# Optimization experiments

Measured on AMD Instinct MI355X. Metric: run time of the kernel, lower is better.

## Reference

```python
import jax, jax.numpy as jnp
import numpy as np


def setup_inputs() -> dict:
    key = jax.random.key(0)
    ks = jax.random.split(key, 8)
    C, dk = 256, 32
    B, H, W = 4, 64, 64
    x = jax.random.normal(ks[0], (B, C, H, W), dtype=jnp.float32)
    wq = jax.random.normal(ks[1], (dk, C), dtype=jnp.float32) * (1.0 / np.sqrt(C))
    bq = jnp.zeros((dk,), dtype=jnp.float32)
    wk = jax.random.normal(ks[2], (dk, C), dtype=jnp.float32) * (1.0 / np.sqrt(C))
    bk = jnp.zeros((dk,), dtype=jnp.float32)
    wv = jax.random.normal(ks[3], (C, C), dtype=jnp.float32) * (1.0 / np.sqrt(C))
    bv = jnp.zeros((C,), dtype=jnp.float32)
    gamma = jnp.ones((1,), dtype=jnp.float32)
    return {"x": x, "wq": wq, "bq": bq, "wk": wk, "bk": bk,
            "wv": wv, "bv": bv, "gamma": gamma}


def reference(x, wq, bq, wk, bk, wv, bv, gamma):
    B, C, H, W = x.shape
    N = H * W
    xf = x.reshape(B, C, N)  # [B, C, N]
    # 1x1 convs == per-pixel linear projections
    q = jnp.einsum('dc,bcn->bnd', wq, xf) + bq  # [B, N, dk]  (proj_query, permuted)
    k = jnp.einsum('dc,bcn->bdn', wk, xf) + bk[None, :, None]  # [B, dk, N]
    v = jnp.einsum('ec,bcn->ben', wv, xf) + bv[None, :, None]  # [B, C, N]
    energy = jnp.einsum('bnd,bdm->bnm', q, k)  # [B, N, N]
    attention = jax.nn.softmax(energy, axis=-1)
    # out[b,c,i] = sum_j v[b,c,j] * attention[b,i,j]
    out = jnp.einsum('bcj,bij->bci', v, attention)  # [B, C, N]
    out = out.reshape(B, C, H, W)
    return gamma[0] * out + x
```

## Files before the change

kernel.cpp:

```cpp
#include <hip/hip_runtime.h>
#include <hip/hip_bf16.h>

#define NPIX 4096
#define CIN  256
#define DK   32

typedef __attribute__((ext_vector_type(8))) short short8;
typedef __attribute__((ext_vector_type(16))) float f32x16;

__device__ __forceinline__ unsigned short f2bf(float f) {
    unsigned int u = __float_as_uint(f);
    return (unsigned short)((u + 0x7fffu + ((u >> 16) & 1u)) >> 16);
}
__device__ __forceinline__ float bf2f(unsigned short h) {
    return __uint_as_float(((unsigned int)h) << 16);
}
__device__ __forceinline__ unsigned int f2bf2(float a, float b) {
    __hip_bfloat162 h = __float22bfloat162_rn(make_float2(a, b));
    unsigned int u;
    __builtin_memcpy(&u, &h, 4);
    return u;
}

__global__ void wprep_kernel(const float* __restrict__ wq, const float* __restrict__ wk,
                             const float* __restrict__ wv,
                             unsigned short* __restrict__ wqh, unsigned short* __restrict__ wql,
                             unsigned short* __restrict__ wkh, unsigned short* __restrict__ wkl,
                             unsigned short* __restrict__ wvh) {
    const int lane = threadIdx.x & 63, li = lane & 31, hi = lane >> 5;
    const int kc = blockIdx.x, y = blockIdx.y;
    if (y < 4) {
        const float* m = (y < 2) ? wq : wk;
        short8 h8, l8;
#pragma unroll
        for (int e = 0; e < 8; ++e) {
            float v = m[li * CIN + kc * 16 + hi * 8 + e];
            unsigned short hb = f2bf(v);
            h8[e] = (short)hb;
            l8[e] = (short)f2bf(v - bf2f(hb));
        }
        unsigned short* dst = (y == 0) ? wqh : (y == 1) ? wql : (y == 2) ? wkh : wkl;
        *reinterpret_cast<short8*>(&dst[kc * 512 + lane * 8]) = (y & 1) ? l8 : h8;
    } else {
        const int cblk = y - 4;
        short8 h8;
#pragma unroll
        for (int e = 0; e < 8; ++e)
            h8[e] = (short)f2bf(wv[(cblk * 32 + li) * CIN + kc * 16 + hi * 8 + e]);
        *reinterpret_cast<short8*>(&wvh[(cblk * 16 + kc) * 512 + lane * 8]) = h8;
    }
}

__global__ __launch_bounds__(512) void projall_kernel(
        const float* __restrict__ x,
        const unsigned short* __restrict__ wqh, const unsigned short* __restrict__ wql,
        const unsigned short* __restrict__ wkh, const unsigned short* __restrict__ wkl,
        const unsigned short* __restrict__ wvh,
        const float* __restrict__ bq, const float* __restrict__ bk, const float* __restrict__ bv,
        unsigned short* __restrict__ qfrag, unsigned short* __restrict__ kfrag,
        unsigned short* __restrict__ vfrag) {
    __shared__ float xs[64][36];
    __shared__ unsigned short xhf[16 * 512];
    __shared__ unsigned short xlf[16 * 512];
    __shared__ unsigned short ts[2][32][40];

    const int t = threadIdx.x, lane = t & 63, li = lane & 31, hi = lane >> 5, w = t >> 6;
    const int nblk = blockIdx.x, b = blockIdx.y;
    const int n0 = nblk * 32;

    for (int cb = 0; cb < 4; ++cb) {
        {
            int c = t >> 3, n4 = (t & 7) * 4;
            float4 v = *reinterpret_cast<const float4*>(
                &x[(size_t)(b * CIN + cb * 64 + c) * NPIX + n0 + n4]);
            xs[c][n4 + 0] = v.x; xs[c][n4 + 1] = v.y;
            xs[c][n4 + 2] = v.z; xs[c][n4 + 3] = v.w;
        }
        __syncthreads();
        {
            const int kc = w & 3;
            const bool isL = (w >= 4);
            short8 f;
#pragma unroll
            for (int e = 0; e < 8; ++e) {
                float v = xs[kc * 16 + hi * 8 + e][li];
                unsigned short hb = f2bf(v);
                f[e] = isL ? (short)f2bf(v - bf2f(hb)) : (short)hb;
            }
            unsigned short* dst = isL ? xlf : xhf;
            *reinterpret_cast<short8*>(&dst[(cb * 4 + kc) * 512 + lane * 8]) = f;
        }
        __syncthreads();
    }

    if (w < 2) {
        const unsigned short* wh = (w == 0) ? wqh : wkh;
        const unsigned short* wl = (w == 0) ? wql : wkl;
        const float* bias = (w == 0) ? bq : bk;
        f32x16 acc;
#pragma unroll
        for (int r = 0; r < 16; ++r) acc[r] = 0.f;
        for (int kc = 0; kc < 16; ++kc) {
            short8 ah = *reinterpret_cast<const short8*>(&xhf[kc * 512 + lane * 8]);
            short8 al = *reinterpret_cast<const short8*>(&xlf[kc * 512 + lane * 8]);
            short8 whf = *reinterpret_cast<const short8*>(&wh[kc * 512 + lane * 8]);
            short8 wlf = *reinterpret_cast<const short8*>(&wl[kc * 512 + lane * 8]);
            acc = __builtin_amdgcn_mfma_f32_32x32x16_bf16(ah, whf, acc, 0, 0, 0);
            acc = __builtin_amdgcn_mfma_f32_32x32x16_bf16(al, whf, acc, 0, 0, 0);
            acc = __builtin_amdgcn_mfma_f32_32x32x16_bf16(ah, wlf, acc, 0, 0, 0);
        }
        const float bs = bias[li];
#pragma unroll
        for (int r = 0; r < 16; ++r) {
            int row = (r & 3) + 8 * (r >> 2) + 4 * hi;
            ts[w][row][li] = f2bf(acc[r] + bs);
        }
        unsigned short* dstf = (w == 0) ? qfrag : kfrag;
#pragma unroll
        for (int dh = 0; dh < 2; ++dh) {
            short8 f = *reinterpret_cast<const short8*>(&ts[w][li][dh * 16 + hi * 8]);
            *reinterpret_cast<short8*>(
                &dstf[((size_t)(b * 128 + nblk) * 2 + dh) * 512 + lane * 8]) = f;
        }
    } else {
        const int w2 = w - 2;
        const int njob = (w2 < 2) ? 2 : 1;
        for (int jj = 0; jj < njob; ++jj) {
            const int cblk = w2 + jj * 6;
            f32x16 acc;
#pragma unroll
            for (int r = 0; r < 16; ++r) acc[r] = 0.f;
            for (int kc = 0; kc < 16; ++kc) {
                short8 xb = *reinterpret_cast<const short8*>(&xhf[kc * 512 + lane * 8]);
                short8 wf = *reinterpret_cast<const short8*>(&wvh[(cblk * 16 + kc) * 512 + lane * 8]);
                acc = __builtin_amdgcn_mfma_f32_32x32x16_bf16(xb, wf, acc, 0, 0, 0);
            }
            const float bvv = bv[cblk * 32 + li];
#pragma unroll
            for (int g = 0; g < 2; ++g) {
                short8 sv;
#pragma unroll
                for (int e = 0; e < 8; ++e) sv[e] = (short)f2bf(acc[g * 8 + e] + bvv);
                *reinterpret_cast<short8*>(
                    &vfrag[((size_t)(b * 8 + cblk) * 256 + nblk * 2 + g) * 512 + lane * 8]) = sv;
            }
        }
    }
}

__global__ __launch_bounds__(512, 4) void attnv_kernel(
        const unsigned short* __restrict__ qfrag, const unsigned short* __restrict__ kfrag,
        const unsigned short* __restrict__ vfrag, unsigned short* __restrict__ opart,
        float* __restrict__ lpart, float* __restrict__ out) {
    __shared__ unsigned short Ps[4 * 8 * 512];
    __shared__ float sred[2][4][32];

    const int t = threadIdx.x, lane = t & 63, li = lane & 31, hi = lane >> 5, w = t >> 6;
    const int blk = blockIdx.x;
    const int xcd = blk & 7, slot = blk >> 3;
    const int jh = slot & 1, ps = slot >> 1;
    const int b = xcd >> 1;
    const int ipos = (xcd & 1) * 32 + ps;

    if (w < 4) {
        const int sl = w;
        short8 qb00, qb01, qb10, qb11;
        {
            size_t q0 = ((size_t)(b * 128 + ipos * 2 + 0) * 2) * 512 + lane * 8;
            size_t q1 = ((size_t)(b * 128 + ipos * 2 + 1) * 2) * 512 + lane * 8;
            qb00 = *reinterpret_cast<const short8*>(&qfrag[q0]);
            qb01 = *reinterpret_cast<const short8*>(&qfrag[q0 + 512]);
            qb10 = *reinterpret_cast<const short8*>(&qfrag[q1]);
            qb11 = *reinterpret_cast<const short8*>(&qfrag[q1 + 512]);
        }
        float ssum0 = 0.f, ssum1 = 0.f;
        short8 kp0, kp1;

        auto kload = [&](int s) {
            size_t koff = ((size_t)(b * 128 + jh * 64 + s * 4 + sl) * 2) * 512 + lane * 8;
            kp0 = *reinterpret_cast<const short8*>(&kfrag[koff]);
            kp1 = *reinterpret_cast<const short8*>(&kfrag[koff + 512]);
        };
        auto eunit = [&](short8 qA, short8 qB, float& ss, int slab, int buf) {
            f32x16 e;
#pragma unroll
            for (int r = 0; r < 16; ++r) e[r] = 0.f;
            e = __builtin_amdgcn_mfma_f32_32x32x16_bf16(kp0, qA, e, 0, 0, 0);
            e = __builtin_amdgcn_mfma_f32_32x32x16_bf16(kp1, qB, e, 0, 0, 0);
#pragma unroll
            for (int g = 0; g < 2; ++g) {
                float p0 = __expf(e[g * 8 + 0]), p1 = __expf(e[g * 8 + 1]);
                float p2 = __expf(e[g * 8 + 2]), p3 = __expf(e[g * 8 + 3]);
                float p4 = __expf(e[g * 8 + 4]), p5 = __expf(e[g * 8 + 5]);
                float p6 = __expf(e[g * 8 + 6]), p7 = __expf(e[g * 8 + 7]);
                ss += ((p0 + p1) + (p2 + p3)) + ((p4 + p5) + (p6 + p7));
                uint4 pk;
                pk.x = f2bf2(p0, p1); pk.y = f2bf2(p2, p3);
                pk.z = f2bf2(p4, p5); pk.w = f2bf2(p6, p7);
                *reinterpret_cast<uint4*>(
                    &Ps[((slab + buf) * 8 + sl * 2 + g) * 512 + lane * 8]) = pk;
            }
        };
        auto do_E2 = [&](int s) {
            const int buf = s & 1;
            eunit(qb00, qb01, ssum0, 0, buf);
            eunit(qb10, qb11, ssum1, 2, buf);
        };

        kload(0);
        do_E2(0);
        kload(1);
        __syncthreads();
#pragma unroll 1
        for (int s = 0; s < 16; ++s) {
            if (s + 1 < 16) {
                do_E2(s + 1);
                if (s + 2 < 16) kload(s + 2);
            }
            __syncthreads();
        }

        ssum0 += __shfl_xor(ssum0, 32);
        ssum1 += __shfl_xor(ssum1, 32);
        if (lane < 32) { sred[0][sl][li] = ssum0; sred[1][sl][li] = ssum1; }
        __syncthreads();
        if (w < 2 && lane < 32) {
            float lt = sred[w][0][li] + sred[w][1][li] + sred[w][2][li] + sred[w][3][li];
            lpart[((size_t)jh * 4 + b) * NPIX + ipos * 64 + w * 32 + li] = lt;
        }
    } else {
        const int cqa = w - 4, cqb = w;
        f32x16 aA0, aA1, aB0, aB1;
#pragma unroll
        for (int r = 0; r < 16; ++r) { aA0[r] = 0.f; aA1[r] = 0.f; aB0[r] = 0.f; aB1[r] = 0.f; }

        short8 vp[8];
        const size_t vbA = ((size_t)(b * 8 + cqa) * 256 + jh * 128) * 512 + lane * 8;
        const size_t vbB = ((size_t)(b * 8 + cqb) * 256 + jh * 128) * 512 + lane * 8;

#pragma unroll
        for (int kc = 0; kc < 8; ++kc)
            vp[kc] = *reinterpret_cast<const short8*>(&vfrag[vbA + kc * 512]);
        __syncthreads();

#pragma unroll 1
        for (int s = 0; s < 16; ++s) {
            const int buf = s & 1;
            {
                const size_t pB = vbB + (size_t)s * 8 * 512;
#pragma unroll
                for (int kc = 0; kc < 8; ++kc) {
                    short8 a = vp[kc];
                    vp[kc] = *reinterpret_cast<const short8*>(&vfrag[pB + kc * 512]);
                    short8 B0 = *reinterpret_cast<const short8*>(&Ps[(buf * 8 + kc) * 512 + lane * 8]);
                    short8 B1 = *reinterpret_cast<const short8*>(&Ps[((2 + buf) * 8 + kc) * 512 + lane * 8]);
                    aA0 = __builtin_amdgcn_mfma_f32_32x32x16_bf16(a, B0, aA0, 0, 0, 0);
                    aA1 = __builtin_amdgcn_mfma_f32_32x32x16_bf16(a, B1, aA1, 0, 0, 0);
                }
            }
            {
                const size_t pA = vbA + (size_t)(s + 1) * 8 * 512;
#pragma unroll
                for (int kc = 0; kc < 8; ++kc) {
                    short8 a = vp[kc];
                    vp[kc] = *reinterpret_cast<const short8*>(&vfrag[pA + kc * 512]);
                    short8 B0 = *reinterpret_cast<const short8*>(&Ps[(buf * 8 + kc) * 512 + lane * 8]);
                    short8 B1 = *reinterpret_cast<const short8*>(&Ps[((2 + buf) * 8 + kc) * 512 + lane * 8]);
                    aB0 = __builtin_amdgcn_mfma_f32_32x32x16_bf16(a, B0, aB0, 0, 0, 0);
                    aB1 = __builtin_amdgcn_mfma_f32_32x32x16_bf16(a, B1, aB1, 0, 0, 0);
                }
            }
            __syncthreads();
        }
        __syncthreads();

#pragma unroll
        for (int cqi = 0; cqi < 2; ++cqi) {
            const int cq = cqi ? cqb : cqa;
#pragma unroll
            for (int itt = 0; itt < 2; ++itt) {
                const f32x16 A = cqi ? (itt ? aB1 : aB0) : (itt ? aA1 : aA0);
#pragma unroll
                for (int r = 0; r < 16; ++r) {
                    int c = cq * 32 + (r & 3) + 8 * (r >> 2) + 4 * hi;
                    size_t idx = (size_t)(b * CIN + c) * NPIX + ipos * 64 + itt * 32 + li;
                    if (jh == 0) out[idx] = A[r];
                    else         opart[idx] = f2bf(A[r]);
                }
            }
        }
    }
}

__global__ __launch_bounds__(256) void merge_kernel(
        const unsigned short* __restrict__ opart, const float* __restrict__ lpart,
        const float* __restrict__ xin, const float* __restrict__ gamma,
        float* __restrict__ out) {
    const size_t idx4 = ((size_t)blockIdx.x * 256 + threadIdx.x) * 4;
    const size_t i  = idx4 & (NPIX - 1);
    const size_t b  = idx4 >> 20;
    float4 o0 = *reinterpret_cast<const float4*>(&out[idx4]);
    float4 xv = *reinterpret_cast<const float4*>(&xin[idx4]);
    float4 l0 = *reinterpret_cast<const float4*>(&lpart[b * NPIX + i]);
    float4 l1 = *reinterpret_cast<const float4*>(&lpart[(4 + b) * NPIX + i]);
    const unsigned short* op = &opart[idx4];
    const float g = gamma[0];
    float4 o;
    o.x = g * (o0.x + bf2f(op[0])) / (l0.x + l1.x) + xv.x;
    o.y = g * (o0.y + bf2f(op[1])) / (l0.y + l1.y) + xv.y;
    o.z = g * (o0.z + bf2f(op[2])) / (l0.z + l1.z) + xv.z;
    o.w = g * (o0.w + bf2f(op[3])) / (l0.w + l1.w) + xv.w;
    *reinterpret_cast<float4*>(&out[idx4]) = o;
}

extern "C" void kernel_launch(void* const* d_in, const int* in_sizes, int n_in,
                              void* d_out, int out_size, void* d_ws, size_t ws_size,
                              hipStream_t stream) {
    const float* x     = (const float*)d_in[0];
    const float* wq    = (const float*)d_in[1];
    const float* bq    = (const float*)d_in[2];
    const float* wk    = (const float*)d_in[3];
    const float* bk    = (const float*)d_in[4];
    const float* wv    = (const float*)d_in[5];
    const float* bv    = (const float*)d_in[6];
    const float* gamma = (const float*)d_in[7];
    float* out = (float*)d_out;

    unsigned short* qf    = (unsigned short*)d_ws;
    unsigned short* kf    = qf + (size_t)524288;
    unsigned short* vf    = kf + (size_t)524288;
    unsigned short* wqh   = vf + (size_t)4194304;
    unsigned short* wql   = wqh + 8192;
    unsigned short* wkh   = wql + 8192;
    unsigned short* wkl   = wkh + 8192;
    unsigned short* wvh   = wkl + 8192;
    unsigned short* opart = wvh + 65536;
    float*          lpart = (float*)(opart + 4194304);

    wprep_kernel<<<dim3(16, 12), 64, 0, stream>>>(wq, wk, wv, wqh, wql, wkh, wkl, wvh);
    projall_kernel<<<dim3(128, 4), 512, 0, stream>>>(x, wqh, wql, wkh, wkl, wvh,
                                                     bq, bk, bv, qf, kf, vf);
    attnv_kernel<<<dim3(512), 512, 0, stream>>>(qf, kf, vf, opart, lpart, out);
    merge_kernel<<<dim3(4096), 256, 0, stream>>>(opart, lpart, x, gamma, out);
}
```

Baseline: 148.9 us.

## Split attention-V channel blocks across two workgroups to double grid size

The attention kernel's grid doubles from 512 to 1024 blocks. Each block now covers half of the 256 output channels, so each consumer wave accumulates one 32-channel block instead of two. Producer waves recompute the QK energies and softmax for each channel half, but only the first half writes the row sums. This buys more parallelism and fewer accumulator registers per wave at the cost of computing the energy/softmax work twice. The merge kernel also reads the bf16 partials with a single vector load instead of four scalar loads.

```diff
diff --git a/kernel.cpp b/kernel.cpp
--- a/kernel.cpp
+++ b/kernel.cpp
@@ -158,7 +158,7 @@
     const int t = threadIdx.x, lane = t & 63, li = lane & 31, hi = lane >> 5, w = t >> 6;
     const int blk = blockIdx.x;
     const int xcd = blk & 7, slot = blk >> 3;
-    const int jh = slot & 1, ps = slot >> 1;
+    const int jh = slot & 1, ps = (slot >> 1) & 31, chalf = slot >> 6;
     const int b = xcd >> 1;
     const int ipos = (xcd & 1) * 32 + ps;
 
@@ -224,69 +224,52 @@
         ssum1 += __shfl_xor(ssum1, 32);
         if (lane < 32) { sred[0][sl][li] = ssum0; sred[1][sl][li] = ssum1; }
         __syncthreads();
-        if (w < 2 && lane < 32) {
+        if (chalf == 0 && w < 2 && lane < 32) {
             float lt = sred[w][0][li] + sred[w][1][li] + sred[w][2][li] + sred[w][3][li];
             lpart[((size_t)jh * 4 + b) * NPIX + ipos * 64 + w * 32 + li] = lt;
         }
     } else {
-        const int cqa = w - 4, cqb = w;
-        f32x16 aA0, aA1, aB0, aB1;
-#pragma unroll
-        for (int r = 0; r < 16; ++r) { aA0[r] = 0.f; aA1[r] = 0.f; aB0[r] = 0.f; aB1[r] = 0.f; }
+        const int cq = chalf * 4 + (w - 4);
+        f32x16 acc0, acc1;
+#pragma unroll
+        for (int r = 0; r < 16; ++r) { acc0[r] = 0.f; acc1[r] = 0.f; }
 
         short8 vp[8];
-        const size_t vbA = ((size_t)(b * 8 + cqa) * 256 + jh * 128) * 512 + lane * 8;
-        const size_t vbB = ((size_t)(b * 8 + cqb) * 256 + jh * 128) * 512 + lane * 8;
-
-#pragma unroll
-        for (int kc = 0; kc < 8; ++kc)
-            vp[kc] = *reinterpret_cast<const short8*>(&vfrag[vbA + kc * 512]);
+        {
+            size_t vb = ((size_t)(b * 8 + cq) * 256 + jh * 128) * 512 + lane * 8;
+#pragma unroll
+            for (int kc = 0; kc < 8; ++kc)
+                vp[kc] = *reinterpret_cast<const short8*>(&vfrag[vb + kc * 512]);
+        }
         __syncthreads();
 
 #pragma unroll 1
         for (int s = 0; s < 16; ++s) {
             const int buf = s & 1;
-            {
-                const size_t pB = vbB + (size_t)s * 8 * 512;
-#pragma unroll
-                for (int kc = 0; kc < 8; ++kc) {
-                    short8 a = vp[kc];
-                    vp[kc] = *reinterpret_cast<const short8*>(&vfrag[pB + kc * 512]);
-                    short8 B0 = *reinterpret_cast<const short8*>(&Ps[(buf * 8 + kc) * 512 + lane * 8]);
-                    short8 B1 = *reinterpret_cast<const short8*>(&Ps[((2 + buf) * 8 + kc) * 512 + lane * 8]);
-                    aA0 = __builtin_amdgcn_mfma_f32_32x32x16_bf16(a, B0, aA0, 0, 0, 0);
-                    aA1 = __builtin_amdgcn_mfma_f32_32x32x16_bf16(a, B1, aA1, 0, 0, 0);
-                }
-            }
-            {
-                const size_t pA = vbA + (size_t)(s + 1) * 8 * 512;
-#pragma unroll
-                for (int kc = 0; kc < 8; ++kc) {
-                    short8 a = vp[kc];
-                    vp[kc] = *reinterpret_cast<const short8*>(&vfrag[pA + kc * 512]);
-                    short8 B0 = *reinterpret_cast<const short8*>(&Ps[(buf * 8 + kc) * 512 + lane * 8]);
-                    short8 B1 = *reinterpret_cast<const short8*>(&Ps[((2 + buf) * 8 + kc) * 512 + lane * 8]);
-                    aB0 = __builtin_amdgcn_mfma_f32_32x32x16_bf16(a, B0, aB0, 0, 0, 0);
-                    aB1 = __builtin_amdgcn_mfma_f32_32x32x16_bf16(a, B1, aB1, 0, 0, 0);
-                }
+            const int spf = (s + 1) & 15;
+            const size_t vbn = ((size_t)(b * 8 + cq) * 256 + jh * 128 + spf * 8) * 512 + lane * 8;
+#pragma unroll
+            for (int kc = 0; kc < 8; ++kc) {
+                short8 a = vp[kc];
+                vp[kc] = *reinterpret_cast<const short8*>(&vfrag[vbn + kc * 512]);
+                short8 B0 = *reinterpret_cast<const short8*>(&Ps[(buf * 8 + kc) * 512 + lane * 8]);
+                short8 B1 = *reinterpret_cast<const short8*>(&Ps[((2 + buf) * 8 + kc) * 512 + lane * 8]);
+                acc0 = __builtin_amdgcn_mfma_f32_32x32x16_bf16(a, B0, acc0, 0, 0, 0);
+                acc1 = __builtin_amdgcn_mfma_f32_32x32x16_bf16(a, B1, acc1, 0, 0, 0);
             }
             __syncthreads();
         }
         __syncthreads();
 
 #pragma unroll
-        for (int cqi = 0; cqi < 2; ++cqi) {
-            const int cq = cqi ? cqb : cqa;
-#pragma unroll
-            for (int itt = 0; itt < 2; ++itt) {
-                const f32x16 A = cqi ? (itt ? aB1 : aB0) : (itt ? aA1 : aA0);
-#pragma unroll
-                for (int r = 0; r < 16; ++r) {
-                    int c = cq * 32 + (r & 3) + 8 * (r >> 2) + 4 * hi;
-                    size_t idx = (size_t)(b * CIN + c) * NPIX + ipos * 64 + itt * 32 + li;
-                    if (jh == 0) out[idx] = A[r];
-                    else         opart[idx] = f2bf(A[r]);
-                }
+        for (int itt = 0; itt < 2; ++itt) {
+            const f32x16& A = itt ? acc1 : acc0;
+#pragma unroll
+            for (int r = 0; r < 16; ++r) {
+                int c = cq * 32 + (r & 3) + 8 * (r >> 2) + 4 * hi;
+                size_t idx = (size_t)(b * CIN + c) * NPIX + ipos * 64 + itt * 32 + li;
+                if (jh == 0) out[idx] = A[r];
+                else         opart[idx] = f2bf(A[r]);
             }
         }
     }
@@ -303,13 +286,13 @@
     float4 xv = *reinterpret_cast<const float4*>(&xin[idx4]);
     float4 l0 = *reinterpret_cast<const float4*>(&lpart[b * NPIX + i]);
     float4 l1 = *reinterpret_cast<const float4*>(&lpart[(4 + b) * NPIX + i]);
-    const unsigned short* op = &opart[idx4];
+    ushort4 opv = *reinterpret_cast<const ushort4*>(&opart[idx4]);
     const float g = gamma[0];
     float4 o;
-    o.x = g * (o0.x + bf2f(op[0])) / (l0.x + l1.x) + xv.x;
-    o.y = g * (o0.y + bf2f(op[1])) / (l0.y + l1.y) + xv.y;
-    o.z = g * (o0.z + bf2f(op[2])) / (l0.z + l1.z) + xv.z;
-    o.w = g * (o0.w + bf2f(op[3])) / (l0.w + l1.w) + xv.w;
+    o.x = g * (o0.x + bf2f(opv.x)) / (l0.x + l1.x) + xv.x;
+    o.y = g * (o0.y + bf2f(opv.y)) / (l0.y + l1.y) + xv.y;
+    o.z = g * (o0.z + bf2f(opv.z)) / (l0.z + l1.z) + xv.z;
+    o.w = g * (o0.w + bf2f(opv.w)) / (l0.w + l1.w) + xv.w;
     *reinterpret_cast<float4*>(&out[idx4]) = o;
 }
 
@@ -340,6 +323,6 @@
     wprep_kernel<<<dim3(16, 12), 64, 0, stream>>>(wq, wk, wv, wqh, wql, wkh, wkl, wvh);
     projall_kernel<<<dim3(128, 4), 512, 0, stream>>>(x, wqh, wql, wkh, wkl, wvh,
                                                      bq, bk, bv, qf, kf, vf);
-    attnv_kernel<<<dim3(512), 512, 0, stream>>>(qf, kf, vf, opart, lpart, out);
+    attnv_kernel<<<dim3(1024), 512, 0, stream>>>(qf, kf, vf, opart, lpart, out);
     merge_kernel<<<dim3(4096), 256, 0, stream>>>(opart, lpart, x, gamma, out);
 }
```

Result: no change. 151.9 us (+2.0%).
